# Kernel tuning notes

Hardware: AMD Instinct MI355X
Metric: run time of the kernel (lower is better)

Reference implementation:

```python
import jax, jax.numpy as jnp
import numpy as np

B, T = 64, 512
EMBED, HIDDEN, NUM_CLASSES = 512, 1024, 256


def setup_inputs() -> dict:
    key = jax.random.key(0)
    ks = jax.random.split(key, 8)
    x = jax.random.randint(ks[0], (B, T), 0, NUM_CLASSES, dtype=jnp.int32)
    # embedding init uniform(-0.1, 0.1) as in the torch module
    embed = jax.random.uniform(ks[1], (NUM_CLASSES, EMBED), minval=-0.1, maxval=0.1, dtype=jnp.float32)
    s_ih = 1.0 / np.sqrt(HIDDEN)
    W_ih = jax.random.uniform(ks[2], (4 * HIDDEN, EMBED), minval=-s_ih, maxval=s_ih, dtype=jnp.float32)
    W_hh = jax.random.uniform(ks[3], (4 * HIDDEN, HIDDEN), minval=-s_ih, maxval=s_ih, dtype=jnp.float32)
    b_ih = jax.random.uniform(ks[4], (4 * HIDDEN,), minval=-s_ih, maxval=s_ih, dtype=jnp.float32)
    b_hh = jax.random.uniform(ks[5], (4 * HIDDEN,), minval=-s_ih, maxval=s_ih, dtype=jnp.float32)
    s_fc = 1.0 / np.sqrt(HIDDEN)
    fc_W = jax.random.uniform(ks[6], (NUM_CLASSES, HIDDEN), minval=-s_fc, maxval=s_fc, dtype=jnp.float32)
    fc_b = jax.random.uniform(ks[7], (NUM_CLASSES,), minval=-s_fc, maxval=s_fc, dtype=jnp.float32)
    return {"x": x, "embed": embed, "W_ih": W_ih, "W_hh": W_hh,
            "b_ih": b_ih, "b_hh": b_hh, "fc_W": fc_W, "fc_b": fc_b}


def _lstm_forward(x, embed, W_ih, W_hh, b_ih, b_hh, fc_W, fc_b):
    H = W_hh.shape[1]
    x_embed = embed[x]                      # [B, T, E]
    # Precompute input-side gate projections for all timesteps at once.
    gates_x = jnp.einsum('bte,ge->btg', x_embed, W_ih) + (b_ih + b_hh)  # [B, T, 4H]
    gates_x = jnp.transpose(gates_x, (1, 0, 2))  # [T, B, 4H]

    def step(carry, g_x):
        h, c = carry
        gates = g_x + h @ W_hh.T            # [B, 4H]
        i, f, g, o = jnp.split(gates, 4, axis=-1)  # torch gate order: i,f,g,o
        i = jax.nn.sigmoid(i)
        f = jax.nn.sigmoid(f)
        g = jnp.tanh(g)
        o = jax.nn.sigmoid(o)
        c = f * c + i * g
        h = o * jnp.tanh(c)
        return (h, c), h

    Bn = x.shape[0]
    h0 = jnp.zeros((Bn, H), dtype=embed.dtype)
    c0 = jnp.zeros((Bn, H), dtype=embed.dtype)
    _, hs = jax.lax.scan(step, (h0, c0), gates_x)   # hs: [T, B, H]
    hs = jnp.transpose(hs, (1, 0, 2))               # [B, T, H]
    out = jnp.einsum('bth,ch->btc', hs, fc_W) + fc_b  # [B, T, C]
    return out


def reference(x, embed, W_ih, W_hh, b_ih, b_hh, fc_W, fc_b):
    return _lstm_forward(x, embed, W_ih, W_hh, b_ih, b_hh, fc_W, fc_b)
```

## Files before the change

### kernel.cpp

```cpp
#include <hip/hip_runtime.h>
#include <math.h>

#define DEV_INLINE __device__ __forceinline__

static constexpr int Bn = 64;
static constexpr int Tn = 512;
static constexpr int En = 512;
static constexpr int Hn = 1024;
static constexpr int Cn = 256;
static constexpr int Gn = 4 * Hn;

typedef float v4f __attribute__((ext_vector_type(4)));
typedef _Float16 v8h __attribute__((ext_vector_type(8)));

DEV_INLINE float sigmoidf_(float v) { return 1.f / (1.f + __expf(-v)); }

__global__ __launch_bounds__(256) void gemm_tt(
    const float* __restrict__ A, const float* __restrict__ Bm,
    const float* __restrict__ bias1, const float* __restrict__ bias2,
    float* __restrict__ Cm, int M, int N, int K)
{
  constexpr int KC = 32;
  __shared__ float As[KC][68];
  __shared__ float Bs[KC][68];
  const int tid = threadIdx.x;
  const int tx = tid & 15, ty = tid >> 4;
  const int m0 = blockIdx.x * 64, n0 = blockIdx.y * 64;

  float acc[4][4] = {};

  for (int k0 = 0; k0 < K; k0 += KC) {
    __syncthreads();
    #pragma unroll
    for (int j = 0; j < 2; ++j) {
      int f = tid + j * 256;
      int row = f >> 3;
      int c4 = f & 7;
      float4 va = *reinterpret_cast<const float4*>(&A[(size_t)(m0 + row) * K + k0 + c4 * 4]);
      As[c4 * 4 + 0][row] = va.x; As[c4 * 4 + 1][row] = va.y;
      As[c4 * 4 + 2][row] = va.z; As[c4 * 4 + 3][row] = va.w;
      float4 vb = *reinterpret_cast<const float4*>(&Bm[(size_t)(n0 + row) * K + k0 + c4 * 4]);
      Bs[c4 * 4 + 0][row] = vb.x; Bs[c4 * 4 + 1][row] = vb.y;
      Bs[c4 * 4 + 2][row] = vb.z; Bs[c4 * 4 + 3][row] = vb.w;
    }
    __syncthreads();
    #pragma unroll
    for (int k = 0; k < KC; ++k) {
      float4 a4 = *reinterpret_cast<const float4*>(&As[k][ty * 4]);
      float4 b4 = *reinterpret_cast<const float4*>(&Bs[k][tx * 4]);
      float ar[4] = {a4.x, a4.y, a4.z, a4.w};
      float br[4] = {b4.x, b4.y, b4.z, b4.w};
      #pragma unroll
      for (int i = 0; i < 4; ++i)
        #pragma unroll
        for (int j = 0; j < 4; ++j)
          acc[i][j] += ar[i] * br[j];
    }
  }

  #pragma unroll
  for (int j = 0; j < 4; ++j) {
    int n = n0 + tx * 4 + j;
    float bb = bias1[n];
    if (bias2) bb += bias2[n];
    #pragma unroll
    for (int i = 0; i < 4; ++i)
      Cm[(size_t)(m0 + ty * 4 + i) * N + n] = acc[i][j] + bb;
  }
}

__global__ __launch_bounds__(256) void gemm_fc(
    const _Float16* __restrict__ A,
    const float* __restrict__ Bm,
    const float* __restrict__ bias,
    float* __restrict__ out)
{
  constexpr int KC = 32;
  __shared__ float As[KC][68];
  __shared__ float Bs[KC][68];
  const int tid = threadIdx.x;
  const int tx = tid & 15, ty = tid >> 4;
  const int m0 = blockIdx.x * 64, n0 = blockIdx.y * 64;

  float acc[4][4] = {};

  for (int k0 = 0; k0 < Hn; k0 += KC) {
    __syncthreads();
    {
      int row = tid >> 2, c8 = tid & 3;
      v8h va = *(const v8h*)(A + (size_t)(m0 + row) * Hn + k0 + c8 * 8);
      #pragma unroll
      for (int e = 0; e < 8; ++e) As[c8 * 8 + e][row] = (float)va[e];
    }
    #pragma unroll
    for (int j = 0; j < 2; ++j) {
      int f = tid + j * 256, row = f >> 3, c4 = f & 7;
      float4 vb = *reinterpret_cast<const float4*>(&Bm[(size_t)(n0 + row) * Hn + k0 + c4 * 4]);
      Bs[c4 * 4 + 0][row] = vb.x; Bs[c4 * 4 + 1][row] = vb.y;
      Bs[c4 * 4 + 2][row] = vb.z; Bs[c4 * 4 + 3][row] = vb.w;
    }
    __syncthreads();
    #pragma unroll
    for (int k = 0; k < KC; ++k) {
      float4 a4 = *reinterpret_cast<const float4*>(&As[k][ty * 4]);
      float4 b4 = *reinterpret_cast<const float4*>(&Bs[k][tx * 4]);
      float ar[4] = {a4.x, a4.y, a4.z, a4.w};
      float br[4] = {b4.x, b4.y, b4.z, b4.w};
      #pragma unroll
      for (int i = 0; i < 4; ++i)
        #pragma unroll
        for (int j = 0; j < 4; ++j)
          acc[i][j] += ar[i] * br[j];
    }
  }

  #pragma unroll
  for (int j = 0; j < 4; ++j) {
    int n = n0 + tx * 4 + j;
    float bb = bias[n];
    #pragma unroll
    for (int i = 0; i < 4; ++i) {
      int m = m0 + ty * 4 + i;
      int b = m & 63, t = m >> 6;
      out[((size_t)b * Tn + t) * Cn + n] = acc[i][j] + bb;
    }
  }
}

__global__ __launch_bounds__(512, 2) void lstm_mfma(
    const int* __restrict__ x,
    const float* __restrict__ Whh,
    const float* __restrict__ proj,
    _Float16* __restrict__ hs16,
    int* __restrict__ flags)
{
  __shared__ __align__(16) char smem[45056];
  char*      hT     = smem;
  float*     gbuf   = (float*)(smem + 32768);
  _Float16*  hstage = (_Float16*)(smem + 43008);

  const int tid = threadIdx.x;
  const int bid = blockIdx.x;
  const int bg = bid >> 5, hg = bid & 31;
  const int b0 = bg * 16;

  const int w = tid >> 6, l = tid & 63;
  const int q = w >> 2, g = w & 3;
  const int mrow = l & 15;
  const int kseg = l >> 4;

  v8h wv[32];
  {
    const float* wr = Whh + (size_t)(g * Hn + hg * 32 + q * 16 + mrow) * Hn + kseg * 8;
    #pragma unroll
    for (int kk = 0; kk < 32; ++kk) {
      const float* p = wr + kk * 32;
      float4 f0 = *(const float4*)p, f1 = *(const float4*)(p + 4);
      v8h h8;
      h8[0] = (_Float16)f0.x; h8[1] = (_Float16)f0.y;
      h8[2] = (_Float16)f0.z; h8[3] = (_Float16)f0.w;
      h8[4] = (_Float16)f1.x; h8[5] = (_Float16)f1.y;
      h8[6] = (_Float16)f1.z; h8[7] = (_Float16)f1.w;
      wv[kk] = h8;
    }
  }

  const int eb = tid >> 5, ehc = tid & 31;
  const int* xp = x + (size_t)(b0 + eb) * Tn;
  float cst = 0.f;

  int* L0  = flags + (size_t)(bg * 6 + (hg >> 3)) * 32;
  int* L1  = flags + (size_t)(bg * 6 + 4) * 32;
  int* GEN = flags + (size_t)(bg * 6 + 5) * 32;

  for (int t = 0; t < Tn; ++t) {
    const int cls = xp[t];
    const float* pb = proj + (size_t)cls * Gn + hg * 32 + ehc;
    float p0 = pb[0], p1 = pb[Hn], p2 = pb[2 * Hn], p3 = pb[3 * Hn];

    if (t > 0) {
      const char* sb = (const char*)(hs16 + ((size_t)(t - 1) * Bn + b0) * Hn);
      const char* a0 = sb + tid * 16;
      const char* a1 = a0 + 8192;
      const char* a2 = a0 + 16384;
      const char* a3 = a0 + 24576;
      v4f r0, r1, r2, r3;
      asm volatile(
        "global_load_dwordx4 %0, %4, off sc0 sc1\n\t"
        "global_load_dwordx4 %1, %5, off sc0 sc1\n\t"
        "global_load_dwordx4 %2, %6, off sc0 sc1\n\t"
        "global_load_dwordx4 %3, %7, off sc0 sc1\n\t"
        "s_waitcnt vmcnt(0)"
        : "=&v"(r0), "=&v"(r1), "=&v"(r2), "=&v"(r3)
        : "v"(a0), "v"(a1), "v"(a2), "v"(a3)
        : "memory");
      v4f rr[4] = {r0, r1, r2, r3};
      #pragma unroll
      for (int i = 0; i < 4; ++i) {
        int fo = tid * 16 + i * 8192;
        int row = fo >> 11, kb = fo & 2047;
        *(v4f*)(hT + row * 2048 + (kb ^ ((row & 7) << 4))) = rr[i];
      }
    }
    __syncthreads();

    v4f acc = {0.f, 0.f, 0.f, 0.f};
    if (t > 0) {
      #pragma unroll
      for (int kk = 0; kk < 32; ++kk) {
        const int kb = kk * 64 + kseg * 16;
        v8h a8 = *(const v8h*)(hT + mrow * 2048 + (kb ^ ((mrow & 7) << 4)));
        acc = __builtin_amdgcn_mfma_f32_16x16x32_f16(a8, wv[kk], acc, 0, 0, 0);
      }
    }

    #pragma unroll
    for (int r = 0; r < 4; ++r)
      gbuf[(g * 32 + q * 16 + mrow) * 20 + kseg * 4 + r] = acc[r];
    __syncthreads();

    {
      float g0 = gbuf[(0 * 32 + ehc) * 20 + eb] + p0;
      float g1 = gbuf[(1 * 32 + ehc) * 20 + eb] + p1;
      float g2 = gbuf[(2 * 32 + ehc) * 20 + eb] + p2;
      float g3 = gbuf[(3 * 32 + ehc) * 20 + eb] + p3;
      float ig = sigmoidf_(g0), fg = sigmoidf_(g1);
      float gg = tanhf(g2),     og = sigmoidf_(g3);
      cst = fg * cst + ig * gg;
      hstage[eb * 32 + ehc] = (_Float16)(og * tanhf(cst));
    }
    __syncthreads();

    if (tid < 64) {
      const int b = tid >> 2, part = tid & 3;
      v4f v = *(const v4f*)(hstage + b * 32 + part * 8);
      _Float16* dp = hs16 + ((size_t)t * Bn + b0 + b) * Hn + hg * 32 + part * 8;
      asm volatile(
        "global_store_dwordx4 %0, %1, off sc0 sc1\n\t"
        "s_waitcnt vmcnt(0)"
        :: "v"(dp), "v"(v) : "memory");
    }

    if (t + 1 < Tn) {
      __syncthreads();
      if (tid == 0) {
        const int t8 = 8 * (t + 1);
        int old = __hip_atomic_fetch_add(L0, 1, __ATOMIC_RELAXED,
                                         __HIP_MEMORY_SCOPE_AGENT);
        if (old == t8 - 1) {
          int o1 = __hip_atomic_fetch_add(L1, 1, __ATOMIC_RELAXED,
                                          __HIP_MEMORY_SCOPE_AGENT);
          if (o1 == 4 * (t + 1) - 1)
            __hip_atomic_store(GEN, t + 1, __ATOMIC_RELAXED,
                               __HIP_MEMORY_SCOPE_AGENT);
        }
        while (__hip_atomic_load(GEN, __ATOMIC_RELAXED,
                                 __HIP_MEMORY_SCOPE_AGENT) < t + 1)
          __builtin_amdgcn_s_sleep(8);
      }
      __syncthreads();
    }
  }
}

extern "C" void kernel_launch(void* const* d_in, const int* in_sizes, int n_in,
                              void* d_out, int out_size, void* d_ws, size_t ws_size,
                              hipStream_t stream) {
  const int*   x     = (const int*)  d_in[0];
  const float* embed = (const float*)d_in[1];
  const float* Wih   = (const float*)d_in[2];
  const float* Whh   = (const float*)d_in[3];
  const float* bih   = (const float*)d_in[4];
  const float* bhh   = (const float*)d_in[5];
  const float* fcW   = (const float*)d_in[6];
  const float* fcb   = (const float*)d_in[7];
  float* out = (float*)d_out;

  char* ws = (char*)d_ws;
  const size_t flagBytes = 32768;
  const size_t projBytes = (size_t)Cn * Gn * sizeof(float);
  const size_t hsBytes   = (size_t)Tn * Bn * Hn * sizeof(_Float16);
  const size_t need = flagBytes + projBytes + hsBytes;
  if (ws_size < need) {
    hipMemsetAsync(d_out, 0, (size_t)out_size * sizeof(float), stream);
    return;
  }
  float*     proj = (float*)(ws + flagBytes);
  _Float16*  hs16 = (_Float16*)(ws + flagBytes + projBytes);

  hipMemsetAsync(d_ws, 0, flagBytes, stream);

  dim3 g1(Cn / 64, Gn / 64);
  gemm_tt<<<g1, 256, 0, stream>>>(embed, Wih, bih, bhh, proj, Cn, Gn, En);

  lstm_mfma<<<128, 512, 0, stream>>>(x, Whh, proj, hs16, (int*)d_ws);

  dim3 g3((Bn * Tn) / 64, Cn / 64);
  gemm_fc<<<g3, 256, 0, stream>>>(hs16, fcW, fcb, out);
}
```

Baseline: 2.303 ms.

## Replace hierarchical atomic barrier with per-step per-block ready flags

Removes the two-level atomic counter barrier and its trailing block-wide syncs. Each block now writes a one-word flag per timestep after storing its hidden-state slice, and consumers poll the 32 flags for their batch group before loading. The hidden-state loads are also rearranged so the LDS tile is already in MFMA operand order, which drops the XOR swizzle, and the gbuf row pitch is padded to 21. The projection loads move after the barrier. The cost is a flag array sized per timestep, 32 polling lanes per block, and possible LDS bank conflicts from the unswizzled layout.

```diff
diff --git a/kernel.cpp b/kernel.cpp
--- a/kernel.cpp
+++ b/kernel.cpp
@@ -134,10 +134,9 @@
     _Float16* __restrict__ hs16,
     int* __restrict__ flags)
 {
-  __shared__ __align__(16) char smem[45056];
-  char*      hT     = smem;
-  float*     gbuf   = (float*)(smem + 32768);
-  _Float16*  hstage = (_Float16*)(smem + 43008);
+  __shared__ __align__(16) char hT[32768];
+  __shared__ float gbuf[128 * 21];
+  __shared__ _Float16 hstage[512];
 
   const int tid = threadIdx.x;
   const int bid = blockIdx.x;
@@ -169,21 +168,26 @@
   const int* xp = x + (size_t)(b0 + eb) * Tn;
   float cst = 0.f;
 
-  int* L0  = flags + (size_t)(bg * 6 + (hg >> 3)) * 32;
-  int* L1  = flags + (size_t)(bg * 6 + 4) * 32;
-  int* GEN = flags + (size_t)(bg * 6 + 5) * 32;
+  const int srcoff = (tid & 15) * 2048 + ((tid >> 4) & 3) * 16 + (tid >> 6) * 64;
 
   for (int t = 0; t < Tn; ++t) {
     const int cls = xp[t];
-    const float* pb = proj + (size_t)cls * Gn + hg * 32 + ehc;
-    float p0 = pb[0], p1 = pb[Hn], p2 = pb[2 * Hn], p3 = pb[3 * Hn];
 
     if (t > 0) {
-      const char* sb = (const char*)(hs16 + ((size_t)(t - 1) * Bn + b0) * Hn);
-      const char* a0 = sb + tid * 16;
-      const char* a1 = a0 + 8192;
-      const char* a2 = a0 + 16384;
-      const char* a3 = a0 + 24576;
+      if (tid < 32) {
+        const int* fp = flags + ((size_t)(t - 1) * 4 + bg) * 32 + tid;
+        int v;
+        do {
+          asm volatile(
+            "global_load_dword %0, %1, off sc0 sc1\n\t"
+            "s_waitcnt vmcnt(0)"
+            : "=v"(v) : "v"(fp) : "memory");
+        } while (v == 0);
+      }
+      __syncthreads();
+
+      const char* src = (const char*)(hs16 + ((size_t)(t - 1) * Bn + b0) * Hn);
+      const char* s0 = src + srcoff;
       v4f r0, r1, r2, r3;
       asm volatile(
         "global_load_dwordx4 %0, %4, off sc0 sc1\n\t"
@@ -192,15 +196,12 @@
         "global_load_dwordx4 %3, %7, off sc0 sc1\n\t"
         "s_waitcnt vmcnt(0)"
         : "=&v"(r0), "=&v"(r1), "=&v"(r2), "=&v"(r3)
-        : "v"(a0), "v"(a1), "v"(a2), "v"(a3)
+        : "v"(s0), "v"(s0 + 512), "v"(s0 + 1024), "v"(s0 + 1536)
         : "memory");
-      v4f rr[4] = {r0, r1, r2, r3};
-      #pragma unroll
-      for (int i = 0; i < 4; ++i) {
-        int fo = tid * 16 + i * 8192;
-        int row = fo >> 11, kb = fo & 2047;
-        *(v4f*)(hT + row * 2048 + (kb ^ ((row & 7) << 4))) = rr[i];
-      }
+      *(v4f*)(hT + tid * 16 +     0) = r0;
+      *(v4f*)(hT + tid * 16 +  8192) = r1;
+      *(v4f*)(hT + tid * 16 + 16384) = r2;
+      *(v4f*)(hT + tid * 16 + 24576) = r3;
     }
     __syncthreads();
 
@@ -208,22 +209,22 @@
     if (t > 0) {
       #pragma unroll
       for (int kk = 0; kk < 32; ++kk) {
-        const int kb = kk * 64 + kseg * 16;
-        v8h a8 = *(const v8h*)(hT + mrow * 2048 + (kb ^ ((mrow & 7) << 4)));
+        v8h a8 = *(const v8h*)(hT + kk * 1024 + l * 16);
         acc = __builtin_amdgcn_mfma_f32_16x16x32_f16(a8, wv[kk], acc, 0, 0, 0);
       }
     }
 
     #pragma unroll
     for (int r = 0; r < 4; ++r)
-      gbuf[(g * 32 + q * 16 + mrow) * 20 + kseg * 4 + r] = acc[r];
+      gbuf[(g * 32 + q * 16 + mrow) * 21 + kseg * 4 + r] = acc[r];
     __syncthreads();
 
     {
-      float g0 = gbuf[(0 * 32 + ehc) * 20 + eb] + p0;
-      float g1 = gbuf[(1 * 32 + ehc) * 20 + eb] + p1;
-      float g2 = gbuf[(2 * 32 + ehc) * 20 + eb] + p2;
-      float g3 = gbuf[(3 * 32 + ehc) * 20 + eb] + p3;
+      const float* pb = proj + (size_t)cls * Gn + hg * 32 + ehc;
+      float g0 = gbuf[(0 * 32 + ehc) * 21 + eb] + pb[0];
+      float g1 = gbuf[(1 * 32 + ehc) * 21 + eb] + pb[Hn];
+      float g2 = gbuf[(2 * 32 + ehc) * 21 + eb] + pb[2 * Hn];
+      float g3 = gbuf[(3 * 32 + ehc) * 21 + eb] + pb[3 * Hn];
       float ig = sigmoidf_(g0), fg = sigmoidf_(g1);
       float gg = tanhf(g2),     og = sigmoidf_(g3);
       cst = fg * cst + ig * gg;
@@ -239,26 +240,14 @@
         "global_store_dwordx4 %0, %1, off sc0 sc1\n\t"
         "s_waitcnt vmcnt(0)"
         :: "v"(dp), "v"(v) : "memory");
-    }
-
-    if (t + 1 < Tn) {
-      __syncthreads();
       if (tid == 0) {
-        const int t8 = 8 * (t + 1);
-        int old = __hip_atomic_fetch_add(L0, 1, __ATOMIC_RELAXED,
-                                         __HIP_MEMORY_SCOPE_AGENT);
-        if (old == t8 - 1) {
-          int o1 = __hip_atomic_fetch_add(L1, 1, __ATOMIC_RELAXED,
-                                          __HIP_MEMORY_SCOPE_AGENT);
-          if (o1 == 4 * (t + 1) - 1)
-            __hip_atomic_store(GEN, t + 1, __ATOMIC_RELAXED,
-                               __HIP_MEMORY_SCOPE_AGENT);
-        }
-        while (__hip_atomic_load(GEN, __ATOMIC_RELAXED,
-                                 __HIP_MEMORY_SCOPE_AGENT) < t + 1)
-          __builtin_amdgcn_s_sleep(8);
+        int one = 1;
+        int* fq = flags + ((size_t)t * 4 + bg) * 32 + hg;
+        asm volatile(
+          "global_store_dword %0, %1, off sc0 sc1\n\t"
+          "s_waitcnt vmcnt(0)"
+          :: "v"(fq), "v"(one) : "memory");
       }
-      __syncthreads();
     }
   }
 }
@@ -277,18 +266,18 @@
   float* out = (float*)d_out;
 
   char* ws = (char*)d_ws;
-  const size_t flagBytes = 32768;
+  const size_t ctlBytes  = (size_t)Tn * 4 * 32 * 4;
   const size_t projBytes = (size_t)Cn * Gn * sizeof(float);
   const size_t hsBytes   = (size_t)Tn * Bn * Hn * sizeof(_Float16);
-  const size_t need = flagBytes + projBytes + hsBytes;
+  const size_t need = ctlBytes + projBytes + hsBytes;
   if (ws_size < need) {
     hipMemsetAsync(d_out, 0, (size_t)out_size * sizeof(float), stream);
     return;
   }
-  float*     proj = (float*)(ws + flagBytes);
-  _Float16*  hs16 = (_Float16*)(ws + flagBytes + projBytes);
-
-  hipMemsetAsync(d_ws, 0, flagBytes, stream);
+  float*     proj = (float*)(ws + ctlBytes);
+  _Float16*  hs16 = (_Float16*)(ws + ctlBytes + projBytes);
+
+  hipMemsetAsync(d_ws, 0, ctlBytes, stream);
 
   dim3 g1(Cn / 64, Gn / 64);
   gemm_tt<<<g1, 256, 0, stream>>>(embed, Wih, bih, bhh, proj, Cn, Gn, En);
```

After: 2.101 ms. 1.1x faster.
